# Kernel tuning notes

Measured on AMD Instinct MI355X. Metric: run time of the kernel, lower is better.

The kernel has to match this reference:

```python
import jax, jax.numpy as jnp
import numpy as np

NUM_CHUNKS = 8
HEAD_DIM = 128
PROJ = 1024       # projection_size (q)
KV_PROJ = 1024    # kv_projection_size
NEG_INF = -1e30


def _rotate_half(x):
    x1, x2 = jnp.split(x, 2, axis=-1)
    return jnp.concatenate((-x2, x1), axis=-1)


def _apply_rope(x, cos, sin):
    # x: [B, S, H, D]; cos/sin: [B, S, 1, rot_dim] with rot_dim == D here
    return x * cos + _rotate_half(x) * sin


def setup_inputs() -> dict:
    key = jax.random.key(0)
    k1, k2, k3 = jax.random.split(key, 3)
    S, B, H = 8192, 1, 1024
    layernorm_output = jax.random.normal(k1, (S, B, H), dtype=jnp.float32)
    # rotary tables, stored [S, 1, 1, rot_dim] (seq-first, like the torch module)
    inv_freq = 1.0 / (10000.0 ** (jnp.arange(0, HEAD_DIM, 2, dtype=jnp.float32) / HEAD_DIM))
    t = jnp.arange(S, dtype=jnp.float32)
    freqs = jnp.einsum('s,d->sd', t, inv_freq)
    emb = jnp.concatenate((freqs, freqs), axis=-1)  # [S, rot_dim]
    freqs_cos = jnp.cos(emb)[:, None, None, :]
    freqs_sin = jnp.sin(emb)[:, None, None, :]
    qkv_weight = jax.random.normal(k2, (PROJ + 2 * KV_PROJ, H), dtype=jnp.float32) * (H ** -0.5)
    qkv_bias = jax.random.normal(k3, (PROJ + 2 * KV_PROJ,), dtype=jnp.float32) * 0.02
    return {
        'layernorm_output': layernorm_output,
        'freqs_cos': freqs_cos,
        'freqs_sin': freqs_sin,
        'qkv_weight': qkv_weight,
        'qkv_bias': qkv_bias,
    }


def reference(layernorm_output, freqs_cos, freqs_sin, qkv_weight, qkv_bias):
    S, B, H = layernorm_output.shape
    cs = S // NUM_CHUNKS  # chunk size
    scale = HEAD_DIM ** -0.5
    # permute(1,0,2,3): [S,1,1,rot] -> [1,S,1,rot] matching [B, seq, head, dim]
    cos = jnp.transpose(freqs_cos, (1, 0, 2, 3))
    sin = jnp.transpose(freqs_sin, (1, 0, 2, 3))

    outs = []
    k_list, v_list = [], []
    for i in range(NUM_CHUNKS):
        st, ed = i * cs, (i + 1) * cs
        x = layernorm_output[st:ed]                      # [cs, B, H]
        qkv = jnp.einsum('sbh,oh->sbo', x, qkv_weight) + qkv_bias
        def to_bshd(t):
            return jnp.transpose(t.reshape(cs, B, -1, HEAD_DIM), (1, 0, 2, 3))
        q = to_bshd(qkv[..., :PROJ])                     # [B, cs, nH, D]
        k = to_bshd(qkv[..., PROJ:PROJ + KV_PROJ])
        v = to_bshd(qkv[..., PROJ + KV_PROJ:])
        cos_i, sin_i = cos[:, st:ed], sin[:, st:ed]
        q = _apply_rope(q, cos_i, sin_i)
        k = _apply_rope(k, cos_i, sin_i)
        k_list.append(k)
        v_list.append(v)

        K = jnp.concatenate(k_list, axis=1)              # [B, (i+1)*cs, nH, D]
        V = jnp.concatenate(v_list, axis=1)
        scores = jnp.einsum('bqhd,bkhd->bhqk', q, K) * scale
        # causal: query global idx st+r attends keys <= st+r; earlier chunks fully visible
        qidx = st + jnp.arange(cs)
        kidx = jnp.arange((i + 1) * cs)
        mask = kidx[None, :] <= qidx[:, None]            # [cs, (i+1)*cs]
        scores = jnp.where(mask[None, None], scores, NEG_INF)
        p = jax.nn.softmax(scores, axis=-1)
        outs.append(jnp.einsum('bhqk,bkhd->bqhd', p, V))
    return jnp.concatenate(outs, axis=1)                 # [B, S, nH, D]
```

## Files before the change

### kernel.cpp

```cpp
#include <hip/hip_runtime.h>
#include <hip/hip_bf16.h>

typedef float f32x4 __attribute__((ext_vector_type(4)));
typedef __bf16 bf16x8 __attribute__((ext_vector_type(8)));
typedef __bf16 bf16x4 __attribute__((ext_vector_type(4)));

#define S_LEN 8192
#define HIDDEN 1024
#define NH 8
#define HD 128

#define QSCALE (0.08838834764831845f * 1.4426950408889634f)
#define FIXMAX 24.0f

__device__ __forceinline__ void async16(const void* g, void* l) {
  __builtin_amdgcn_global_load_lds(
      (const __attribute__((address_space(1))) char*)g,
      (__attribute__((address_space(3))) char*)l, 16, 0, 0);
}

__global__ void cast_bf16_kernel(const float* __restrict__ in, __bf16* __restrict__ out) {
  int i = (blockIdx.x * blockDim.x + threadIdx.x) * 4;
  float4 v = *(const float4*)(in + i);
  bf16x4 o;
  o[0] = (__bf16)v.x; o[1] = (__bf16)v.y; o[2] = (__bf16)v.z; o[3] = (__bf16)v.w;
  *(bf16x4*)(out + i) = o;
}

__global__ __launch_bounds__(256) void gemm_qkv(
    const __bf16* __restrict__ A, const __bf16* __restrict__ W,
    const float* __restrict__ bias,
    __bf16* __restrict__ Qb, __bf16* __restrict__ Kb, __bf16* __restrict__ Vt)
{
  __shared__ __bf16 As[128 * 32];
  __shared__ __bf16 Bs[128 * 32];
  const int t = threadIdx.x;
  const int lane = t & 63;
  const int w = t >> 6;
  const int wy = w >> 1, wx = w & 1;
  const int quad = lane >> 4, l15 = lane & 15;
  const int m0 = blockIdx.y * 128;
  const int n0 = blockIdx.x * 128;
  f32x4 acc[4][4] = {};
  for (int kt = 0; kt < HIDDEN; kt += 32) {
#pragma unroll
    for (int j = 0; j < 2; ++j) {
      int idx = j * 256 + t;
      int row = idx >> 2, c8 = (idx & 3) * 8;
      async16(A + (size_t)(m0 + row) * HIDDEN + kt + c8, As + idx * 8);
      async16(W + (size_t)(n0 + row) * HIDDEN + kt + c8, Bs + idx * 8);
    }
    __syncthreads();
    bf16x8 af[4], bfr[4];
#pragma unroll
    for (int i = 0; i < 4; ++i)
      af[i] = *(const bf16x8*)(As + (wy * 64 + i * 16 + l15) * 32 + quad * 8);
#pragma unroll
    for (int i = 0; i < 4; ++i)
      bfr[i] = *(const bf16x8*)(Bs + (wx * 64 + i * 16 + l15) * 32 + quad * 8);
#pragma unroll
    for (int mt = 0; mt < 4; ++mt)
#pragma unroll
      for (int nt = 0; nt < 4; ++nt)
        acc[mt][nt] = __builtin_amdgcn_mfma_f32_16x16x32_bf16(af[mt], bfr[nt], acc[mt][nt], 0, 0, 0);
    __syncthreads();
  }
  float bv[4];
  int cols[4];
#pragma unroll
  for (int nt = 0; nt < 4; ++nt) {
    cols[nt] = n0 + wx * 64 + nt * 16 + l15;
    bv[nt] = bias[cols[nt]];
  }
#pragma unroll
  for (int mt = 0; mt < 4; ++mt) {
    int srow_base = m0 + wy * 64 + mt * 16 + quad * 4;
#pragma unroll
    for (int nt = 0; nt < 4; ++nt) {
      int c = cols[nt];
#pragma unroll
      for (int r = 0; r < 4; ++r) {
        int s = srow_base + r;
        __bf16 b = (__bf16)(acc[mt][nt][r] + bv[nt]);
        if (n0 < 1024) {
          int h = c >> 7, d = c & 127;
          Qb[(size_t)h * S_LEN * HD + (size_t)s * HD + d] = b;
        } else if (n0 < 2048) {
          int c2 = c - 1024; int h = c2 >> 7, d = c2 & 127;
          Kb[(size_t)h * S_LEN * HD + (size_t)s * HD + d] = b;
        } else {
          int c2 = c - 2048; int h = c2 >> 7, d = c2 & 127;
          Vt[(size_t)h * HD * S_LEN + (size_t)d * S_LEN + s] = b;
        }
      }
    }
  }
}

__global__ void rope_kernel(__bf16* __restrict__ Qb, __bf16* __restrict__ Kb,
                            const float* __restrict__ fcos, const float* __restrict__ fsin)
{
  int gid = blockIdx.x * blockDim.x + threadIdx.x;
  int d = gid & 63;
  int h = (gid >> 6) & 7;
  int s = gid >> 9;
  float c1 = fcos[s * 128 + d],      s1 = fsin[s * 128 + d];
  float c2 = fcos[s * 128 + d + 64], s2 = fsin[s * 128 + d + 64];
  size_t base = (size_t)h * S_LEN * HD + (size_t)s * HD + d;
  float q1 = (float)Qb[base], q2 = (float)Qb[base + 64];
  Qb[base]      = (__bf16)((q1 * c1 - q2 * s1) * QSCALE);
  Qb[base + 64] = (__bf16)((q2 * c2 + q1 * s2) * QSCALE);
  float k1 = (float)Kb[base], k2 = (float)Kb[base + 64];
  Kb[base]      = (__bf16)(k1 * c1 - k2 * s1);
  Kb[base + 64] = (__bf16)(k2 * c2 + k1 * s2);
}

__global__ __launch_bounds__(256, 3) void attn_kernel(
    const __bf16* __restrict__ Qb, const __bf16* __restrict__ Kb,
    const __bf16* __restrict__ Vt, float* __restrict__ out,
    __bf16* __restrict__ partO, float* __restrict__ partML)
{
  __shared__ __bf16 Ks[2][32 * 128];
  __shared__ __bf16 Vs[2][64 * 64];
  const int t = threadIdx.x;
  const int lane = t & 63, w = t >> 6;
  const int quad = lane >> 4, l15 = lane & 15;
  const int sw = l15 & 7;

  const int id = blockIdx.x;
  const int k = id / 24, r = id % 24;
  int head, qi, piece, j0, j1;
  bool isPartial;
  if (r < 16) { qi = 63 - k; piece = r >> 3; head = r & 7;
                j0 = piece * (2 * qi + 2); j1 = j0 + (2 * qi + 2); isPartial = true; }
  else        { qi = 31 - k; piece = 0; head = r - 16;
                j0 = 0; j1 = 4 * qi + 4; isPartial = false; }
  const int qs = qi * 128;
  const int jmax_w = 4 * qi + w;
  const __bf16* Qh = Qb + (size_t)head * S_LEN * HD;
  const __bf16* Kh = Kb + (size_t)head * S_LEN * HD;
  const __bf16* Vh = Vt + (size_t)head * HD * S_LEN;

  bf16x8 qf[2][4];
#pragma unroll
  for (int qg = 0; qg < 2; ++qg) {
    int qrow = qs + w * 32 + qg * 16 + l15;
#pragma unroll
    for (int dk = 0; dk < 4; ++dk)
      qf[qg][dk] = *(const bf16x8*)(Qh + (size_t)qrow * HD + dk * 32 + quad * 8);
  }

  f32x4 o[2][8] = {};
  float l_loc[2] = {0.f, 0.f};
  const f32x4 FM = {-FIXMAX, -FIXMAX, -FIXMAX, -FIXMAX};

  auto stageK = [&](int j, int sel) {
    const __bf16* Kp = Kh + (size_t)(j * 32) * HD;
    __bf16* Kd = &Ks[sel][0];
#pragma unroll
    for (int li = 0; li < 2; ++li) {
      int slot = li * 256 + t;
      int kr = slot >> 4, cp = slot & 15;
      async16(Kp + (size_t)kr * HD + (cp ^ (kr & 7)) * 8, Kd + slot * 8);
    }
  };
  auto stageV = [&](int j, int sel) {
    const __bf16* Vp = Vh + j * 32;
    __bf16* Vd = &Vs[sel][0];
#pragma unroll
    for (int li = 0; li < 2; ++li) {
      int c = li * 256 + t;
      int rr = c >> 3, sl = c & 7;
      int slu = sl ^ (rr & 7);
      int d = 2 * rr + (slu >> 2);
      async16(Vp + (size_t)d * S_LEN + (slu & 3) * 8, Vd + c * 8);
    }
  };

  stageK(j0, 0);
  stageV(j0, 0);

  for (int j = j0; j < j1; ++j) {
    const int cur = (j - j0) & 1;
    __builtin_amdgcn_s_barrier();
    asm volatile("" ::: "memory");
    const bool pf_next = (j + 1 < j1);
    if (pf_next) {
      stageK(j + 1, cur ^ 1);
      stageV(j + 1, cur ^ 1);
    }
    if (pf_next) asm volatile("s_waitcnt vmcnt(4)" ::: "memory");
    else         asm volatile("s_waitcnt vmcnt(0)" ::: "memory");
    __builtin_amdgcn_sched_barrier(0);
    __builtin_amdgcn_s_barrier();
    asm volatile("" ::: "memory");

    if (j > jmax_w) continue;
    const __bf16* Ksb = &Ks[cur][0];
    const __bf16* Vsb = &Vs[cur][0];

    f32x4 sc[2][2];
#pragma unroll
    for (int mtk = 0; mtk < 2; ++mtk) {
      bf16x8 kf = *(const bf16x8*)(Ksb + (mtk * 16 + l15) * 128 + ((quad ^ sw) * 8));
      sc[0][mtk] = __builtin_amdgcn_mfma_f32_16x16x32_bf16(kf, qf[0][0], FM, 0, 0, 0);
      sc[1][mtk] = __builtin_amdgcn_mfma_f32_16x16x32_bf16(kf, qf[1][0], FM, 0, 0, 0);
    }
#pragma unroll
    for (int dk = 1; dk < 4; ++dk)
#pragma unroll
      for (int mtk = 0; mtk < 2; ++mtk) {
        bf16x8 kf = *(const bf16x8*)(Ksb + (mtk * 16 + l15) * 128 + (((dk * 4 + quad) ^ sw) * 8));
        sc[0][mtk] = __builtin_amdgcn_mfma_f32_16x16x32_bf16(kf, qf[0][dk], sc[0][mtk], 0, 0, 0);
        sc[1][mtk] = __builtin_amdgcn_mfma_f32_16x16x32_bf16(kf, qf[1][dk], sc[1][mtk], 0, 0, 0);
      }

    if (j == jmax_w) {
#pragma unroll
      for (int qg = 0; qg < 2; ++qg)
#pragma unroll
        for (int mtk = 0; mtk < 2; ++mtk)
#pragma unroll
          for (int r2 = 0; r2 < 4; ++r2)
            if (mtk * 16 + quad * 4 + r2 > qg * 16 + l15)
              sc[qg][mtk][r2] = -1e30f;
    }

    bf16x8 pf[2];
#pragma unroll
    for (int qg = 0; qg < 2; ++qg) {
      float p[2][4];
#pragma unroll
      for (int mtk = 0; mtk < 2; ++mtk)
#pragma unroll
        for (int r2 = 0; r2 < 4; ++r2) {
          p[mtk][r2] = __builtin_amdgcn_exp2f(sc[qg][mtk][r2]);
          l_loc[qg] += p[mtk][r2];
        }
      unsigned u0, u1, v0, v1;
      asm("v_cvt_pk_bf16_f32 %0, %1, %2" : "=v"(u0) : "v"(p[0][0]), "v"(p[0][1]));
      asm("v_cvt_pk_bf16_f32 %0, %1, %2" : "=v"(u1) : "v"(p[0][2]), "v"(p[0][3]));
      asm("v_cvt_pk_bf16_f32 %0, %1, %2" : "=v"(v0) : "v"(p[1][0]), "v"(p[1][1]));
      asm("v_cvt_pk_bf16_f32 %0, %1, %2" : "=v"(v1) : "v"(p[1][2]), "v"(p[1][3]));
      asm("v_permlane32_swap_b32 %0, %1" : "+v"(u0), "+v"(v0));
      asm("v_permlane32_swap_b32 %0, %1" : "+v"(u1), "+v"(v1));
      asm("v_permlane16_swap_b32 %0, %1" : "+v"(u0), "+v"(v0));
      asm("v_permlane16_swap_b32 %0, %1" : "+v"(u1), "+v"(v1));
      union { unsigned r4[4]; bf16x8 v8; } pu;
      pu.r4[0] = u0; pu.r4[1] = u1; pu.r4[2] = v0; pu.r4[3] = v1;
      pf[qg] = pu.v8;
    }

#pragma unroll
    for (int dt = 0; dt < 8; ++dt) {
      int d = dt * 16 + l15;
      int rr = d >> 1;
      int slu = ((d & 1) << 2) | quad;
      bf16x8 vf = *(const bf16x8*)(Vsb + rr * 64 + ((slu ^ (rr & 7)) * 8));
      o[0][dt] = __builtin_amdgcn_mfma_f32_16x16x32_bf16(vf, pf[0], o[0][dt], 0, 0, 0);
      o[1][dt] = __builtin_amdgcn_mfma_f32_16x16x32_bf16(vf, pf[1], o[1][dt], 0, 0, 0);
    }
  }

  float inv[2], lfull[2];
#pragma unroll
  for (int qg = 0; qg < 2; ++qg) {
    float lv = l_loc[qg];
    lv += __shfl_xor(lv, 16);
    lv += __shfl_xor(lv, 32);
    lfull[qg] = lv;
    inv[qg] = 1.0f / lv;
  }
  if (!isPartial) {
#pragma unroll
    for (int qg = 0; qg < 2; ++qg) {
      int s = qs + w * 32 + qg * 16 + l15;
#pragma unroll
      for (int dt = 0; dt < 8; ++dt) {
        f32x4 v;
#pragma unroll
        for (int r2 = 0; r2 < 4; ++r2) v[r2] = o[qg][dt][r2] * inv[qg];
        *(f32x4*)(out + (size_t)s * 1024 + head * 128 + dt * 16 + quad * 4) = v;
      }
    }
  } else {
    int u = (qi - 32) * 16 + piece * 8 + head;
    __bf16* Op = partO + (size_t)u * 128 * 128;
    float* mlp = partML + u * 256;
#pragma unroll
    for (int qg = 0; qg < 2; ++qg) {
      int row = w * 32 + qg * 16 + l15;
#pragma unroll
      for (int dt = 0; dt < 8; ++dt) {
        bf16x4 pk;
#pragma unroll
        for (int r2 = 0; r2 < 4; ++r2) pk[r2] = (__bf16)(o[qg][dt][r2] * inv[qg]);
        *(bf16x4*)(Op + row * 128 + dt * 16 + quad * 4) = pk;
      }
    }
    if (quad == 0) {
#pragma unroll
      for (int qg = 0; qg < 2; ++qg)
        mlp[w * 32 + qg * 16 + l15] = lfull[qg];
    }
  }
}

__global__ __launch_bounds__(256) void merge_kernel(
    const __bf16* __restrict__ partO, const float* __restrict__ partML,
    float* __restrict__ out)
{
  int b = blockIdx.x;
  int qi = 32 + (b >> 3), head = b & 7;
  int u0 = (qi - 32) * 16 + head;
  int u1 = u0 + 8;
  int t = threadIdx.x;
  int q = t >> 1, dh = (t & 1) * 64;
  float l0 = partML[u0 * 256 + q];
  float l1 = partML[u1 * 256 + q];
  float inv = 1.0f / (l0 + l1);
  float w0 = l0 * inv, w1 = l1 * inv;
  const __bf16* O0 = partO + ((size_t)u0 * 128 + q) * 128 + dh;
  const __bf16* O1 = partO + ((size_t)u1 * 128 + q) * 128 + dh;
  float* op = out + (size_t)(qi * 128 + q) * 1024 + head * 128 + dh;
#pragma unroll
  for (int d = 0; d < 64; d += 8) {
    bf16x8 a = *(const bf16x8*)(O0 + d);
    bf16x8 c = *(const bf16x8*)(O1 + d);
    float4 r0, r1;
    r0.x = w0 * (float)a[0] + w1 * (float)c[0];
    r0.y = w0 * (float)a[1] + w1 * (float)c[1];
    r0.z = w0 * (float)a[2] + w1 * (float)c[2];
    r0.w = w0 * (float)a[3] + w1 * (float)c[3];
    r1.x = w0 * (float)a[4] + w1 * (float)c[4];
    r1.y = w0 * (float)a[5] + w1 * (float)c[5];
    r1.z = w0 * (float)a[6] + w1 * (float)c[6];
    r1.w = w0 * (float)a[7] + w1 * (float)c[7];
    *(float4*)(op + d) = r0;
    *(float4*)(op + d + 4) = r1;
  }
}

extern "C" void kernel_launch(void* const* d_in, const int* in_sizes, int n_in,
                              void* d_out, int out_size, void* d_ws, size_t ws_size,
                              hipStream_t stream)
{
  const float* x    = (const float*)d_in[0];
  const float* fcos = (const float*)d_in[1];
  const float* fsin = (const float*)d_in[2];
  const float* wq   = (const float*)d_in[3];
  const float* bias = (const float*)d_in[4];
  float* out = (float*)d_out;

  char* ws = (char*)d_ws;
  __bf16* xb = (__bf16*)ws;
  __bf16* wb = (__bf16*)(ws + 16777216);
  __bf16* Qb = (__bf16*)(ws + 23068672);
  __bf16* Kb = (__bf16*)(ws + 39845888);
  __bf16* Vt = (__bf16*)(ws + 56623104);

  __bf16* partO = xb;
  float* partML = (float*)wb;

  cast_bf16_kernel<<<8192, 256, 0, stream>>>(x, xb);
  cast_bf16_kernel<<<3072, 256, 0, stream>>>(wq, wb);
  dim3 gg(24, 64);
  gemm_qkv<<<gg, 256, 0, stream>>>(xb, wb, bias, Qb, Kb, Vt);
  rope_kernel<<<16384, 256, 0, stream>>>(Qb, Kb, fcos, fsin);
  attn_kernel<<<768, 256, 0, stream>>>(Qb, Kb, Vt, out, partO, partML);
  merge_kernel<<<256, 256, 0, stream>>>(partO, partML, out);
}
```

Before: 373.2 us.

## Fuse RoPE and Q scaling into QKV GEMM epilogue, vectorize V-transpose stores

Removes the separate rope kernel. The GEMM's B-tile column mapping is remapped so each thread holds both halves (d and d+64) of a head dimension, which lets RoPE and the Q scale be applied directly in the epilogue before the single bf16 store. The V-transpose output is now written as packed 4-element bf16 vectors along the sequence axis. This saves one read-modify-write pass over Q and K and one launch, at the cost of extra cos/sin global loads inside the GEMM epilogue.

```diff
diff --git a/kernel.cpp b/kernel.cpp
--- a/kernel.cpp
+++ b/kernel.cpp
@@ -30,6 +30,7 @@
 __global__ __launch_bounds__(256) void gemm_qkv(
     const __bf16* __restrict__ A, const __bf16* __restrict__ W,
     const float* __restrict__ bias,
+    const float* __restrict__ fcos, const float* __restrict__ fsin,
     __bf16* __restrict__ Qb, __bf16* __restrict__ Kb, __bf16* __restrict__ Vt)
 {
   __shared__ __bf16 As[128 * 32];
@@ -57,7 +58,7 @@
       af[i] = *(const bf16x8*)(As + (wy * 64 + i * 16 + l15) * 32 + quad * 8);
 #pragma unroll
     for (int i = 0; i < 4; ++i)
-      bfr[i] = *(const bf16x8*)(Bs + (wx * 64 + i * 16 + l15) * 32 + quad * 8);
+      bfr[i] = *(const bf16x8*)(Bs + (i * 32 + wx * 16 + l15) * 32 + quad * 8);
 #pragma unroll
     for (int mt = 0; mt < 4; ++mt)
 #pragma unroll
@@ -66,53 +67,48 @@
     __syncthreads();
   }
   float bv[4];
-  int cols[4];
-#pragma unroll
-  for (int nt = 0; nt < 4; ++nt) {
-    cols[nt] = n0 + wx * 64 + nt * 16 + l15;
-    bv[nt] = bias[cols[nt]];
-  }
-#pragma unroll
-  for (int mt = 0; mt < 4; ++mt) {
-    int srow_base = m0 + wy * 64 + mt * 16 + quad * 4;
-#pragma unroll
-    for (int nt = 0; nt < 4; ++nt) {
-      int c = cols[nt];
-#pragma unroll
-      for (int r = 0; r < 4; ++r) {
-        int s = srow_base + r;
-        __bf16 b = (__bf16)(acc[mt][nt][r] + bv[nt]);
-        if (n0 < 1024) {
-          int h = c >> 7, d = c & 127;
-          Qb[(size_t)h * S_LEN * HD + (size_t)s * HD + d] = b;
-        } else if (n0 < 2048) {
-          int c2 = c - 1024; int h = c2 >> 7, d = c2 & 127;
-          Kb[(size_t)h * S_LEN * HD + (size_t)s * HD + d] = b;
-        } else {
-          int c2 = c - 2048; int h = c2 >> 7, d = c2 & 127;
-          Vt[(size_t)h * HD * S_LEN + (size_t)d * S_LEN + s] = b;
+#pragma unroll
+  for (int nt = 0; nt < 4; ++nt)
+    bv[nt] = bias[n0 + nt * 32 + wx * 16 + l15];
+
+  if (n0 < 2048) {
+    const bool isQ = (n0 < 1024);
+    const int h = (isQ ? n0 : n0 - 1024) >> 7;
+    __bf16* Out = (isQ ? Qb : Kb) + (size_t)h * S_LEN * HD;
+    const float qsc = isQ ? QSCALE : 1.0f;
+#pragma unroll
+    for (int mt = 0; mt < 4; ++mt) {
+      int srow_base = m0 + wy * 64 + mt * 16 + quad * 4;
+#pragma unroll
+      for (int np = 0; np < 2; ++np) {
+        int d = np * 32 + wx * 16 + l15;
+#pragma unroll
+        for (int r = 0; r < 4; ++r) {
+          int s = srow_base + r;
+          float c1 = fcos[s * 128 + d],      s1 = fsin[s * 128 + d];
+          float c2 = fcos[s * 128 + d + 64], s2 = fsin[s * 128 + d + 64];
+          float a1 = acc[mt][np][r] + bv[np];
+          float a2 = acc[mt][np + 2][r] + bv[np + 2];
+          Out[(size_t)s * HD + d]      = (__bf16)((a1 * c1 - a2 * s1) * qsc);
+          Out[(size_t)s * HD + d + 64] = (__bf16)((a2 * c2 + a1 * s2) * qsc);
         }
       }
     }
-  }
-}
-
-__global__ void rope_kernel(__bf16* __restrict__ Qb, __bf16* __restrict__ Kb,
-                            const float* __restrict__ fcos, const float* __restrict__ fsin)
-{
-  int gid = blockIdx.x * blockDim.x + threadIdx.x;
-  int d = gid & 63;
-  int h = (gid >> 6) & 7;
-  int s = gid >> 9;
-  float c1 = fcos[s * 128 + d],      s1 = fsin[s * 128 + d];
-  float c2 = fcos[s * 128 + d + 64], s2 = fsin[s * 128 + d + 64];
-  size_t base = (size_t)h * S_LEN * HD + (size_t)s * HD + d;
-  float q1 = (float)Qb[base], q2 = (float)Qb[base + 64];
-  Qb[base]      = (__bf16)((q1 * c1 - q2 * s1) * QSCALE);
-  Qb[base + 64] = (__bf16)((q2 * c2 + q1 * s2) * QSCALE);
-  float k1 = (float)Kb[base], k2 = (float)Kb[base + 64];
-  Kb[base]      = (__bf16)(k1 * c1 - k2 * s1);
-  Kb[base + 64] = (__bf16)(k2 * c2 + k1 * s2);
+  } else {
+    const int h = (n0 - 2048) >> 7;
+#pragma unroll
+    for (int mt = 0; mt < 4; ++mt) {
+      int srow_base = m0 + wy * 64 + mt * 16 + quad * 4;
+#pragma unroll
+      for (int nt = 0; nt < 4; ++nt) {
+        int d = nt * 32 + wx * 16 + l15;
+        bf16x4 pk;
+#pragma unroll
+        for (int r = 0; r < 4; ++r) pk[r] = (__bf16)(acc[mt][nt][r] + bv[nt]);
+        *(bf16x4*)(Vt + (size_t)h * HD * S_LEN + (size_t)d * S_LEN + srow_base) = pk;
+      }
+    }
+  }
 }
 
 __global__ __launch_bounds__(256, 3) void attn_kernel(
@@ -365,8 +361,7 @@
   cast_bf16_kernel<<<8192, 256, 0, stream>>>(x, xb);
   cast_bf16_kernel<<<3072, 256, 0, stream>>>(wq, wb);
   dim3 gg(24, 64);
-  gemm_qkv<<<gg, 256, 0, stream>>>(xb, wb, bias, Qb, Kb, Vt);
-  rope_kernel<<<16384, 256, 0, stream>>>(Qb, Kb, fcos, fsin);
+  gemm_qkv<<<gg, 256, 0, stream>>>(xb, wb, bias, fcos, fsin, Qb, Kb, Vt);
   attn_kernel<<<768, 256, 0, stream>>>(Qb, Kb, Vt, out, partO, partML);
   merge_kernel<<<256, 256, 0, stream>>>(partO, partML, out);
 }
```

Result: faster. 362.5 us (-2.9%).
